# Kernel tuning notes

Hardware: AMD Instinct MI355X
Metric: run time of the kernel (lower is better)

## Reference

```python
import jax, jax.numpy as jnp
import numpy as np

NUM_HEADS = 16
ROTARY_BASE = 10000.0


def _apply_rotary(x):
    # x: (B, S, H, D); GPT-NeoX style rotate-half over full head dim
    B, S, H, D = x.shape
    half = D // 2
    inv_freq = 1.0 / (ROTARY_BASE ** (jnp.arange(0, half, dtype=jnp.float32) / half))
    t = jnp.arange(S, dtype=jnp.float32)
    freqs = jnp.einsum('s,d->sd', t, inv_freq)          # (S, half)
    cos = jnp.cos(freqs)[None, :, None, :]               # (1, S, 1, half)
    sin = jnp.sin(freqs)[None, :, None, :]
    x1, x2 = x[..., :half], x[..., half:]
    return jnp.concatenate([x1 * cos - x2 * sin, x2 * cos + x1 * sin], axis=-1).astype(x.dtype)


def setup_inputs() -> dict:
    key = jax.random.key(0)
    k0, k1, k2 = jax.random.split(key, 3)
    B, S, E = 2, 2048, 2048
    x = jax.random.normal(k0, (B, S, E), dtype=jnp.float32)
    wqkv = jax.random.normal(k1, (3 * E, E), dtype=jnp.float32) * 0.02
    bqkv = jnp.zeros((3 * E,), dtype=jnp.float32)
    wout = jax.random.normal(k2, (E, E), dtype=jnp.float32) * 0.02
    bout = jnp.zeros((E,), dtype=jnp.float32)
    return {"x": x, "wqkv": wqkv, "bqkv": bqkv, "wout": wout, "bout": bout}


def reference(x, wqkv, bqkv, wout, bout):
    B, S, E = x.shape
    H = NUM_HEADS
    D = E // H
    # fused QKV projection: (B, S, 3, H, D)
    qkv = (jnp.einsum('bse,fe->bsf', x, wqkv) + bqkv).reshape(B, S, 3, H, D)
    q, k, v = qkv[:, :, 0], qkv[:, :, 1], qkv[:, :, 2]
    q = _apply_rotary(q)
    k = _apply_rotary(k)
    scale = 1.0 / jnp.sqrt(jnp.float32(D))
    scores = jnp.einsum('bthd,bshd->bhts', q, k) * scale  # (B, H, S, S)
    causal_mask = jnp.triu(jnp.full((S, S), -10000.0, dtype=scores.dtype), 1)
    attn = jax.nn.softmax(scores + causal_mask, axis=-1)
    ctx = jnp.einsum('bhts,bshd->bthd', attn, v).reshape(B, S, E)
    return jnp.einsum('bse,fe->bsf', ctx, wout) + bout
```

## Files before the change

kernel.cpp:

```cpp
#include <hip/hip_runtime.h>
#include <math.h>

#define BB 2
#define SS 2048
#define EE 2048
#define HH 16
#define DD 128
#define FF 6144

typedef __attribute__((ext_vector_type(8))) short short8;
typedef __attribute__((ext_vector_type(4))) float floatx4;

static __device__ __forceinline__ unsigned short f2bf(float x) {
  unsigned u = __float_as_uint(x);
  u += 0x7fffu + ((u >> 16) & 1u);
  return (unsigned short)(u >> 16);
}
static __device__ __forceinline__ float bf2f(unsigned short h) {
  return __uint_as_float((unsigned)h << 16);
}

#define GLOAD_LDS16(gp, lp)                                       \
  __builtin_amdgcn_global_load_lds(                               \
      (const __attribute__((address_space(1))) void*)(gp),        \
      (__attribute__((address_space(3))) void*)(lp), 16, 0, 0)

__global__ __launch_bounds__(256) void cast_f32_bf16(
    const float* __restrict__ in, unsigned short* __restrict__ out, int n4) {
  const int i = blockIdx.x * 256 + threadIdx.x;
  if (i >= n4) return;
  const float4 v = ((const float4*)in)[i];
  ushort4 o;
  o.x = f2bf(v.x); o.y = f2bf(v.y); o.z = f2bf(v.z); o.w = f2bf(v.w);
  ((ushort4*)out)[i] = o;
}

static __device__ __forceinline__ void store_out(float* p, float v) { *p = v; }
static __device__ __forceinline__ void store_out(unsigned short* p, float v) {
  *p = f2bf(v);
}

template <typename OutT>
__global__ __launch_bounds__(256) void gemm_bf16_mfma(
    const unsigned short* __restrict__ A, const unsigned short* __restrict__ Bt,
    const float* __restrict__ bias, OutT* __restrict__ C,
    int M, int N, int K) {
  __shared__ unsigned short As[2][128][32];
  __shared__ unsigned short Bs[2][128][32];
  const int tid = threadIdx.x;
  const int L = tid & 63;
  const int w = tid >> 6;
  const int m0 = blockIdx.y * 128;
  const int n0 = blockIdx.x * 128;

  const int i0 = w * 2;
  const int lrow = L >> 2;
  const int lcol = (L & 3) * 8;
  const size_t a_off0 = (size_t)(m0 + (i0 + 0) * 16 + lrow) * K + lcol;
  const size_t a_off1 = (size_t)(m0 + (i0 + 1) * 16 + lrow) * K + lcol;
  const size_t b_off0 = (size_t)(n0 + (i0 + 0) * 16 + lrow) * K + lcol;
  const size_t b_off1 = (size_t)(n0 + (i0 + 1) * 16 + lrow) * K + lcol;

  const int wr = (w >> 1) * 64;
  const int wc = (w & 1) * 64;
  const int lane16 = L & 15;
  const int quad = L >> 4;

  floatx4 acc[4][4] = {};

  GLOAD_LDS16(A + a_off0, &As[0][(i0 + 0) * 16][0]);
  GLOAD_LDS16(A + a_off1, &As[0][(i0 + 1) * 16][0]);
  GLOAD_LDS16(Bt + b_off0, &Bs[0][(i0 + 0) * 16][0]);
  GLOAD_LDS16(Bt + b_off1, &Bs[0][(i0 + 1) * 16][0]);

  for (int k0 = 0; k0 < K; k0 += 32) {
    const int cur = (k0 >> 5) & 1;
    __syncthreads();
    if (k0 + 32 < K) {
      const int nxt = cur ^ 1;
      GLOAD_LDS16(A + a_off0 + k0 + 32, &As[nxt][(i0 + 0) * 16][0]);
      GLOAD_LDS16(A + a_off1 + k0 + 32, &As[nxt][(i0 + 1) * 16][0]);
      GLOAD_LDS16(Bt + b_off0 + k0 + 32, &Bs[nxt][(i0 + 0) * 16][0]);
      GLOAD_LDS16(Bt + b_off1 + k0 + 32, &Bs[nxt][(i0 + 1) * 16][0]);
    }

    short8 a[4], b[4];
#pragma unroll
    for (int mi = 0; mi < 4; ++mi)
      a[mi] = *(const short8*)(&As[cur][wr + mi * 16 + lane16][quad * 8]);
#pragma unroll
    for (int ni = 0; ni < 4; ++ni)
      b[ni] = *(const short8*)(&Bs[cur][wc + ni * 16 + lane16][quad * 8]);
#pragma unroll
    for (int mi = 0; mi < 4; ++mi)
#pragma unroll
      for (int ni = 0; ni < 4; ++ni)
        acc[mi][ni] = __builtin_amdgcn_mfma_f32_16x16x32_bf16(
            a[mi], b[ni], acc[mi][ni], 0, 0, 0);
  }

#pragma unroll
  for (int ni = 0; ni < 4; ++ni) {
    const int col = n0 + wc + ni * 16 + lane16;
    const float bv = bias[col];
#pragma unroll
    for (int mi = 0; mi < 4; ++mi) {
      const int row = m0 + wr + mi * 16 + quad * 4;
#pragma unroll
      for (int r = 0; r < 4; ++r)
        store_out(&C[(size_t)(row + r) * N + col], acc[mi][ni][r] + bv);
    }
  }
}

template <typename OutT>
__global__ __launch_bounds__(512, 2) void gemm_bf16_256x192(
    const unsigned short* __restrict__ A, const unsigned short* __restrict__ Bt,
    const float* __restrict__ bias, OutT* __restrict__ C,
    int M, int N, int K) {
  __shared__ __align__(16) unsigned short As[2][16384];
  __shared__ __align__(16) unsigned short Bs[2][12288];

  const int tid = threadIdx.x;
  const int w = tid >> 6;
  const int L = tid & 63;
  const int lane16 = L & 15;
  const int quad = L >> 4;
  const int wm = w >> 2;
  const int wn = w & 3;

  const int nby = M >> 8;
  const int q8 = gridDim.x >> 3;
  const int wg = (blockIdx.x & 7) * q8 + (blockIdx.x >> 3);
  const int by = wg % nby;
  const int bx = wg / nby;
  const int m0 = by << 8;
  const int n0 = bx * 192;

  const int lA = ((w >> 1) << 4) + (L >> 2);
  const int scol = ((w & 1) << 5) + (((L & 3) * 8) ^ ((L & 32) ? 16 : 0));
  unsigned aoff[4], boff[3];
#pragma unroll
  for (int j = 0; j < 4; ++j)
    aoff[j] = (unsigned)(m0 + j * 64 + lA) * (unsigned)K + scol;
#pragma unroll
  for (int j = 0; j < 3; ++j)
    boff[j] = (unsigned)(n0 + j * 64 + lA) * (unsigned)K + scol;
  const int ldst = w * 512;

  const int sq = (quad * 8) ^ ((lane16 & 8) << 1);
  const int rbase = lane16 * 32 + sq;

  floatx4 acc[8][3] = {};

  GLOAD_LDS16(A + aoff[0], &As[0][0 * 4096 + ldst]);
  GLOAD_LDS16(A + aoff[1], &As[0][1 * 4096 + ldst]);
  GLOAD_LDS16(A + aoff[2], &As[0][2 * 4096 + ldst]);
  GLOAD_LDS16(A + aoff[3], &As[0][3 * 4096 + ldst]);
  GLOAD_LDS16(Bt + boff[0], &Bs[0][0 * 4096 + ldst]);
  GLOAD_LDS16(Bt + boff[1], &Bs[0][1 * 4096 + ldst]);
  GLOAD_LDS16(Bt + boff[2], &Bs[0][2 * 4096 + ldst]);
  GLOAD_LDS16(Bt + boff[0] + 64, &Bs[1][0 * 4096 + ldst]);
  GLOAD_LDS16(Bt + boff[1] + 64, &Bs[1][1 * 4096 + ldst]);
  GLOAD_LDS16(Bt + boff[2] + 64, &Bs[1][2 * 4096 + ldst]);
  asm volatile("s_waitcnt vmcnt(3)" ::: "memory");
  __builtin_amdgcn_sched_barrier(0);
  __builtin_amdgcn_s_barrier();

  const int NT = K >> 6;
  short8 a[4][2], b[3][2];

  for (int t = 0; t < NT; ++t) {
    const int c = t & 1;
    const unsigned kn1 = (unsigned)(t + 1) << 6;
    const unsigned kn2 = (unsigned)(t + 2) << 6;
    const unsigned short* Ac = &As[c][0];
    const unsigned short* Bc = &Bs[c][0];

#pragma unroll
    for (int mi = 0; mi < 4; ++mi)
#pragma unroll
      for (int kk = 0; kk < 2; ++kk)
        a[mi][kk] = *(const short8*)(Ac + (wm * 2) * 4096 +
                                     ((mi * 2 + kk) * 512) + rbase);
#pragma unroll
    for (int ni = 0; ni < 3; ++ni) {
      const int f = wn * 3 + ni;
#pragma unroll
      for (int kk = 0; kk < 2; ++kk)
        b[ni][kk] = *(const short8*)(Bc + (f >> 2) * 4096 +
                                     (((f & 3) * 2 + kk) * 512) + rbase);
    }
    GLOAD_LDS16(A + aoff[0] + kn1, &As[c ^ 1][0 * 4096 + ldst]);
    GLOAD_LDS16(A + aoff[1] + kn1, &As[c ^ 1][1 * 4096 + ldst]);
    GLOAD_LDS16(A + aoff[2] + kn1, &As[c ^ 1][2 * 4096 + ldst]);
    GLOAD_LDS16(A + aoff[3] + kn1, &As[c ^ 1][3 * 4096 + ldst]);
    __builtin_amdgcn_s_setprio(1);
#pragma unroll
    for (int mi = 0; mi < 4; ++mi)
#pragma unroll
      for (int ni = 0; ni < 3; ++ni)
#pragma unroll
        for (int kk = 0; kk < 2; ++kk)
          acc[mi][ni] = __builtin_amdgcn_mfma_f32_16x16x32_bf16(
              a[mi][kk], b[ni][kk], acc[mi][ni], 0, 0, 0);
    __builtin_amdgcn_s_setprio(0);
    __builtin_amdgcn_sched_barrier(0);
    __builtin_amdgcn_s_barrier();

#pragma unroll
    for (int mi = 0; mi < 4; ++mi)
#pragma unroll
      for (int kk = 0; kk < 2; ++kk)
        a[mi][kk] = *(const short8*)(Ac + (wm * 2 + 1) * 4096 +
                                     ((mi * 2 + kk) * 512) + rbase);
    GLOAD_LDS16(Bt + boff[0] + kn2, &Bs[c][0 * 4096 + ldst]);
    GLOAD_LDS16(Bt + boff[1] + kn2, &Bs[c][1 * 4096 + ldst]);
    GLOAD_LDS16(Bt + boff[2] + kn2, &Bs[c][2 * 4096 + ldst]);
    __builtin_amdgcn_s_setprio(1);
#pragma unroll
    for (int mi = 0; mi < 4; ++mi)
#pragma unroll
      for (int ni = 0; ni < 3; ++ni)
#pragma unroll
        for (int kk = 0; kk < 2; ++kk)
          acc[4 + mi][ni] = __builtin_amdgcn_mfma_f32_16x16x32_bf16(
              a[mi][kk], b[ni][kk], acc[4 + mi][ni], 0, 0, 0);
    __builtin_amdgcn_s_setprio(0);
    asm volatile("s_waitcnt vmcnt(3)" ::: "memory");
    __builtin_amdgcn_sched_barrier(0);
    __builtin_amdgcn_s_barrier();
  }

#pragma unroll
  for (int ni = 0; ni < 3; ++ni) {
    const int col = n0 + wn * 48 + ni * 16 + lane16;
    const float bv = bias[col];
#pragma unroll
    for (int mi = 0; mi < 8; ++mi) {
      const int row = m0 + wm * 128 + mi * 16 + quad * 4;
#pragma unroll
      for (int r = 0; r < 4; ++r)
        store_out(&C[(size_t)(row + r) * N + col], acc[mi][ni][r] + bv);
    }
  }
}

__global__ __launch_bounds__(256) void rotary_kernel(unsigned short* __restrict__ qkv) {
  const int idx = blockIdx.x * blockDim.x + threadIdx.x;
  const int d = idx & 63;
  const int h = (idx >> 6) & (HH - 1);
  const int s = (idx >> 10) & (SS - 1);
  const int b = idx >> 21;

  const float inv_freq = __expf(-(float)d * 0.14391156509f);
  float sn, c;
  __sincosf((float)s * inv_freq, &sn, &c);

  const size_t base = ((size_t)b * SS + s) * FF + h * DD + d;
  unsigned short* q = qkv + base;
  unsigned short* k = qkv + base + EE;

  const float q1 = bf2f(q[0]), q2 = bf2f(q[64]);
  q[0]  = f2bf(q1 * c - q2 * sn);
  q[64] = f2bf(q2 * c + q1 * sn);
  const float k1 = bf2f(k[0]), k2 = bf2f(k[64]);
  k[0]  = f2bf(k1 * c - k2 * sn);
  k[64] = f2bf(k2 * c + k1 * sn);
}

__global__ __launch_bounds__(256) void transpose_v(
    const unsigned short* __restrict__ qkv, unsigned short* __restrict__ vt) {
  __shared__ unsigned short T[64][72];
  const int t = threadIdx.x;
  const int s0 = blockIdx.x * 64;
  const int d0 = blockIdx.y * 64;
  const int bh = blockIdx.z;
  const int b = bh >> 4, h = bh & 15;
  {
    const int r = t >> 2, c = (t & 3) * 16;
    const unsigned short* src =
        qkv + ((size_t)b * SS + s0 + r) * FF + 2 * EE + h * DD + d0 + c;
    const uint4 u0 = *(const uint4*)src;
    const uint4 u1 = *(const uint4*)(src + 8);
    *(uint4*)&T[r][c] = u0;
    *(uint4*)&T[r][c + 8] = u1;
  }
  __syncthreads();
  {
    const int rr = t >> 2, cc = (t & 3) * 16;
    unsigned short vals[16];
#pragma unroll
    for (int j = 0; j < 16; ++j) vals[j] = T[cc + j][rr];
    unsigned short* dst =
        vt + (size_t)bh * DD * SS + (size_t)(d0 + rr) * SS + s0 + cc;
    *(uint4*)dst = *(uint4*)&vals[0];
    *(uint4*)(dst + 8) = *(uint4*)&vals[8];
  }
}

#define ATQ 128
#define ATK 32
#define SPAD 40
#define NQT (SS / ATQ)

__global__ __launch_bounds__(256, 2) void attn_mfma(
    const unsigned short* __restrict__ qkv,
    const unsigned short* __restrict__ vt,
    unsigned short* __restrict__ ctx) {
  __shared__ __align__(16) unsigned short Ksh[2][ATK * DD];
  __shared__ __align__(16) unsigned short Vsh[2][DD * ATK];
  __shared__ __align__(16) unsigned short Ssh[ATQ][SPAD];

  const int tid = threadIdx.x;
  const int L = tid & 63;
  const int w = tid >> 6;
  const int lane16 = L & 15;
  const int quad = L >> 4;

  const int flat = blockIdx.x;
  const int bh_lin = flat & 31;
  const int qb = (NQT - 1) - (flat >> 5);
  const int b = bh_lin >> 4;
  const int h = bh_lin & 15;
  const int bh = b * HH + h;
  const float scale = 0.08838834764831845f;

  size_t koff[2], voff[2];
  int kdst[2], vdst[2];
#pragma unroll
  for (int j = 0; j < 2; ++j) {
    const int ck = j * 256 + tid;
    const int kk = ck >> 4;
    const int cgk = (ck & 15) ^ (kk & 15);
    koff[j] = ((size_t)b * SS + kk) * FF + EE + h * DD + cgk * 8;
    kdst[j] = (j * 256 + w * 64) * 8;
    const int d = ck >> 2;
    const int cgv = (ck & 3) ^ (d & 3);
    voff[j] = (size_t)bh * DD * SS + (size_t)d * SS + cgv * 8;
    vdst[j] = kdst[j];
  }

  const int q0 = qb * ATQ;

  short8 qf[2][4];
#pragma unroll
  for (int mi = 0; mi < 2; ++mi) {
    const int q = q0 + w * 32 + mi * 16 + lane16;
    const unsigned short* qp =
        qkv + ((size_t)b * SS + q) * FF + h * DD + quad * 8;
#pragma unroll
    for (int dc = 0; dc < 4; ++dc)
      qf[mi][dc] = *(const short8*)(qp + dc * 32);
  }

  floatx4 acc[8][2] = {};
  float m_i[2] = {-3.0e38f, -3.0e38f};
  float l_i[2] = {0.0f, 0.0f};

  const int nkt = 4 * qb + 4;
  const int mykt = 4 * qb + w;

#pragma unroll
  for (int j = 0; j < 2; ++j) {
    GLOAD_LDS16(qkv + koff[j], &Ksh[0][kdst[j]]);
    GLOAD_LDS16(vt + voff[j], &Vsh[0][vdst[j]]);
  }

  for (int kt = 0; kt < nkt; ++kt) {
    const int cur = kt & 1;
    __syncthreads();
    if (kt + 1 < nkt) {
      const size_t ka = (size_t)(kt + 1) * ATK * FF;
      const int va = (kt + 1) * ATK;
#pragma unroll
      for (int j = 0; j < 2; ++j) {
        GLOAD_LDS16(qkv + koff[j] + ka, &Ksh[cur ^ 1][kdst[j]]);
        GLOAD_LDS16(vt + voff[j] + va, &Vsh[cur ^ 1][vdst[j]]);
      }
    }
    if (kt > mykt) continue;
    const int k0 = kt * ATK;
    const unsigned short* Kc = Ksh[cur];
    const unsigned short* Vc = Vsh[cur];

    floatx4 st[2][2] = {};
    __builtin_amdgcn_s_setprio(1);
#pragma unroll
    for (int kkt = 0; kkt < 2; ++kkt) {
      const unsigned short* krow = Kc + (kkt * 16 + lane16) * 128;
#pragma unroll
      for (int dc = 0; dc < 4; ++dc) {
        const short8 kf =
            *(const short8*)(krow + ((dc * 4 + quad) ^ lane16) * 8);
#pragma unroll
        for (int mi = 0; mi < 2; ++mi)
          st[kkt][mi] = __builtin_amdgcn_mfma_f32_16x16x32_bf16(
              kf, qf[mi][dc], st[kkt][mi], 0, 0, 0);
      }
    }
    __builtin_amdgcn_s_setprio(0);

    const bool needmask = (kt == mykt);
#pragma unroll
    for (int mi = 0; mi < 2; ++mi) {
      const int q_glob = q0 + w * 32 + mi * 16 + lane16;
#pragma unroll
      for (int kkt = 0; kkt < 2; ++kkt) {
        const int kkb = k0 + kkt * 16 + quad * 4;
#pragma unroll
        for (int r = 0; r < 4; ++r) {
          float v = st[kkt][mi][r] * scale;
          if (needmask && (kkb + r) > q_glob) v = -3.0e38f;
          st[kkt][mi][r] = v;
        }
      }
    }

#pragma unroll
    for (int mi = 0; mi < 2; ++mi) {
      float tm = -3.0e38f;
#pragma unroll
      for (int kkt = 0; kkt < 2; ++kkt)
#pragma unroll
        for (int r = 0; r < 4; ++r) tm = fmaxf(tm, st[kkt][mi][r]);
      tm = fmaxf(tm, __shfl_xor(tm, 16));
      tm = fmaxf(tm, __shfl_xor(tm, 32));

      const bool need = !__all(tm - m_i[mi] <= 8.0f);
      if (need) {
        const float mn = fmaxf(m_i[mi], tm);
        const float alpha = __expf(m_i[mi] - mn);
        m_i[mi] = mn;
        l_i[mi] *= alpha;
#pragma unroll
        for (int dt = 0; dt < 8; ++dt)
#pragma unroll
          for (int r = 0; r < 4; ++r) acc[dt][mi][r] *= alpha;
      }

      float rs = 0.0f;
#pragma unroll
      for (int kkt = 0; kkt < 2; ++kkt)
#pragma unroll
        for (int r = 0; r < 4; ++r) {
          const float p = __expf(st[kkt][mi][r] - m_i[mi]);
          st[kkt][mi][r] = p;
          rs += p;
        }
      rs += __shfl_xor(rs, 16);
      rs += __shfl_xor(rs, 32);
      l_i[mi] += rs;

#pragma unroll
      for (int kkt = 0; kkt < 2; ++kkt) {
        ushort4 pk;
        pk.x = f2bf(st[kkt][mi][0]);
        pk.y = f2bf(st[kkt][mi][1]);
        pk.z = f2bf(st[kkt][mi][2]);
        pk.w = f2bf(st[kkt][mi][3]);
        *(ushort4*)(&Ssh[w * 32 + mi * 16 + lane16][kkt * 16 + quad * 4]) = pk;
      }
    }

    short8 pa[2];
#pragma unroll
    for (int mi = 0; mi < 2; ++mi)
      pa[mi] = *(const short8*)(&Ssh[w * 32 + mi * 16 + lane16][quad * 8]);
    const int vpos = (quad ^ (lane16 & 3)) * 8;
    __builtin_amdgcn_s_setprio(1);
#pragma unroll
    for (int dt = 0; dt < 8; ++dt) {
      const short8 vf = *(const short8*)(Vc + (dt * 16 + lane16) * 32 + vpos);
#pragma unroll
      for (int mi = 0; mi < 2; ++mi)
        acc[dt][mi] = __builtin_amdgcn_mfma_f32_16x16x32_bf16(
            vf, pa[mi], acc[dt][mi], 0, 0, 0);
    }
    __builtin_amdgcn_s_setprio(0);
  }

#pragma unroll
  for (int mi = 0; mi < 2; ++mi) {
    const float inv = 1.0f / l_i[mi];
    const int q = q0 + w * 32 + mi * 16 + lane16;
    unsigned short* op = ctx + ((size_t)b * SS + q) * EE + h * DD + quad * 4;
#pragma unroll
    for (int dt = 0; dt < 8; ++dt) {
      ushort4 o;
      o.x = f2bf(acc[dt][mi][0] * inv);
      o.y = f2bf(acc[dt][mi][1] * inv);
      o.z = f2bf(acc[dt][mi][2] * inv);
      o.w = f2bf(acc[dt][mi][3] * inv);
      *(ushort4*)(op + dt * 16) = o;
    }
  }
}

extern "C" void kernel_launch(void* const* d_in, const int* in_sizes, int n_in,
                              void* d_out, int out_size, void* d_ws,
                              size_t ws_size, hipStream_t stream) {
  const float* x    = (const float*)d_in[0];
  const float* wqkv = (const float*)d_in[1];
  const float* bqkv = (const float*)d_in[2];
  const float* wout = (const float*)d_in[3];
  const float* bout = (const float*)d_in[4];
  float* out = (float*)d_out;

  unsigned short* qkvb = (unsigned short*)d_ws;
  unsigned short* xb   = qkvb + (size_t)25165824;
  unsigned short* wqb  = xb + (size_t)8388608;
  unsigned short* ctxb = wqb + (size_t)12582912;
  unsigned short* wob  = ctxb + (size_t)8388608;
  unsigned short* vtb  = wob + (size_t)4194304;

  const int M = BB * SS;

  cast_f32_bf16<<<8192, 256, 0, stream>>>(x, xb, 2097152);
  cast_f32_bf16<<<12288, 256, 0, stream>>>(wqkv, wqb, 3145728);
  cast_f32_bf16<<<4096, 256, 0, stream>>>(wout, wob, 1048576);

  {
    gemm_bf16_256x192<unsigned short><<<dim3(512), 512, 0, stream>>>(
        xb, wqb, bqkv, qkvb, M, FF, EE);
  }
  {
    const int total = BB * SS * HH * 64;
    rotary_kernel<<<total / 256, 256, 0, stream>>>(qkvb);
  }
  {
    dim3 grid(SS / 64, DD / 64, BB * HH);
    transpose_v<<<grid, 256, 0, stream>>>(qkvb, vtb);
  }
  {
    attn_mfma<<<dim3(512), 256, 0, stream>>>(qkvb, vtb, ctxb);
  }
  {
    dim3 grid(EE / 128, M / 128);
    gemm_bf16_mfma<float><<<grid, 256, 0, stream>>>(
        ctxb, wob, bout, out, M, EE, EE);
  }
}
```

Baseline: 419.9 us.

## Use 512-thread attention with 16 rows per wave and a new 256x128 output GEMM

The attention kernel now runs 512 threads per block, each wave owning 16 query rows instead of 32, with one K/V load per thread per tile. The goal is more waves per CU and lower register pressure, at the cost of loading K/V fragments for fewer rows each. The output projection drops the simple 128x128 GEMM for a new 256x128 kernel with swizzled LDS, split-phase prefetch, grouped block ordering and setprio. That kernel should raise MFMA utilization on the 4096x2048x2048 GEMM.

Measured after the change: 398.3 us. -5.2%, faster.

```diff
diff --git a/kernel.cpp b/kernel.cpp
--- a/kernel.cpp
+++ b/kernel.cpp
@@ -38,79 +38,6 @@
 static __device__ __forceinline__ void store_out(float* p, float v) { *p = v; }
 static __device__ __forceinline__ void store_out(unsigned short* p, float v) {
   *p = f2bf(v);
-}
-
-template <typename OutT>
-__global__ __launch_bounds__(256) void gemm_bf16_mfma(
-    const unsigned short* __restrict__ A, const unsigned short* __restrict__ Bt,
-    const float* __restrict__ bias, OutT* __restrict__ C,
-    int M, int N, int K) {
-  __shared__ unsigned short As[2][128][32];
-  __shared__ unsigned short Bs[2][128][32];
-  const int tid = threadIdx.x;
-  const int L = tid & 63;
-  const int w = tid >> 6;
-  const int m0 = blockIdx.y * 128;
-  const int n0 = blockIdx.x * 128;
-
-  const int i0 = w * 2;
-  const int lrow = L >> 2;
-  const int lcol = (L & 3) * 8;
-  const size_t a_off0 = (size_t)(m0 + (i0 + 0) * 16 + lrow) * K + lcol;
-  const size_t a_off1 = (size_t)(m0 + (i0 + 1) * 16 + lrow) * K + lcol;
-  const size_t b_off0 = (size_t)(n0 + (i0 + 0) * 16 + lrow) * K + lcol;
-  const size_t b_off1 = (size_t)(n0 + (i0 + 1) * 16 + lrow) * K + lcol;
-
-  const int wr = (w >> 1) * 64;
-  const int wc = (w & 1) * 64;
-  const int lane16 = L & 15;
-  const int quad = L >> 4;
-
-  floatx4 acc[4][4] = {};
-
-  GLOAD_LDS16(A + a_off0, &As[0][(i0 + 0) * 16][0]);
-  GLOAD_LDS16(A + a_off1, &As[0][(i0 + 1) * 16][0]);
-  GLOAD_LDS16(Bt + b_off0, &Bs[0][(i0 + 0) * 16][0]);
-  GLOAD_LDS16(Bt + b_off1, &Bs[0][(i0 + 1) * 16][0]);
-
-  for (int k0 = 0; k0 < K; k0 += 32) {
-    const int cur = (k0 >> 5) & 1;
-    __syncthreads();
-    if (k0 + 32 < K) {
-      const int nxt = cur ^ 1;
-      GLOAD_LDS16(A + a_off0 + k0 + 32, &As[nxt][(i0 + 0) * 16][0]);
-      GLOAD_LDS16(A + a_off1 + k0 + 32, &As[nxt][(i0 + 1) * 16][0]);
-      GLOAD_LDS16(Bt + b_off0 + k0 + 32, &Bs[nxt][(i0 + 0) * 16][0]);
-      GLOAD_LDS16(Bt + b_off1 + k0 + 32, &Bs[nxt][(i0 + 1) * 16][0]);
-    }
-
-    short8 a[4], b[4];
-#pragma unroll
-    for (int mi = 0; mi < 4; ++mi)
-      a[mi] = *(const short8*)(&As[cur][wr + mi * 16 + lane16][quad * 8]);
-#pragma unroll
-    for (int ni = 0; ni < 4; ++ni)
-      b[ni] = *(const short8*)(&Bs[cur][wc + ni * 16 + lane16][quad * 8]);
-#pragma unroll
-    for (int mi = 0; mi < 4; ++mi)
-#pragma unroll
-      for (int ni = 0; ni < 4; ++ni)
-        acc[mi][ni] = __builtin_amdgcn_mfma_f32_16x16x32_bf16(
-            a[mi], b[ni], acc[mi][ni], 0, 0, 0);
-  }
-
-#pragma unroll
-  for (int ni = 0; ni < 4; ++ni) {
-    const int col = n0 + wc + ni * 16 + lane16;
-    const float bv = bias[col];
-#pragma unroll
-    for (int mi = 0; mi < 4; ++mi) {
-      const int row = m0 + wr + mi * 16 + quad * 4;
-#pragma unroll
-      for (int r = 0; r < 4; ++r)
-        store_out(&C[(size_t)(row + r) * N + col], acc[mi][ni][r] + bv);
-    }
-  }
 }
 
 template <typename OutT>
@@ -246,6 +173,136 @@
   }
 }
 
+template <typename OutT>
+__global__ __launch_bounds__(512, 2) void gemm_bf16_256x128(
+    const unsigned short* __restrict__ A, const unsigned short* __restrict__ Bt,
+    const float* __restrict__ bias, OutT* __restrict__ C,
+    int M, int N, int K) {
+  __shared__ __align__(16) unsigned short As[2][16384];
+  __shared__ __align__(16) unsigned short Bs[2][8192];
+
+  const int tid = threadIdx.x;
+  const int w = tid >> 6;
+  const int L = tid & 63;
+  const int lane16 = L & 15;
+  const int quad = L >> 4;
+  const int wm = w >> 2;
+  const int wn = w & 3;
+
+  const int nby = M >> 8;
+  const int q8 = gridDim.x >> 3;
+  const int wg = (blockIdx.x & 7) * q8 + (blockIdx.x >> 3);
+  const int by = wg % nby;
+  const int bx = wg / nby;
+  const int m0 = by << 8;
+  const int n0 = bx << 7;
+
+  const int lA = ((w >> 1) << 4) + (L >> 2);
+  const int scol = ((w & 1) << 5) + (((L & 3) * 8) ^ ((L & 32) ? 16 : 0));
+  unsigned aoff[4], boff[2];
+#pragma unroll
+  for (int j = 0; j < 4; ++j)
+    aoff[j] = (unsigned)(m0 + j * 64 + lA) * (unsigned)K + scol;
+#pragma unroll
+  for (int j = 0; j < 2; ++j)
+    boff[j] = (unsigned)(n0 + j * 64 + lA) * (unsigned)K + scol;
+  const int ldst = w * 512;
+
+  const int sq = (quad * 8) ^ ((lane16 & 8) << 1);
+  const int rbase = lane16 * 32 + sq;
+
+  floatx4 acc[8][2] = {};
+
+  GLOAD_LDS16(A + aoff[0], &As[0][0 * 4096 + ldst]);
+  GLOAD_LDS16(A + aoff[1], &As[0][1 * 4096 + ldst]);
+  GLOAD_LDS16(A + aoff[2], &As[0][2 * 4096 + ldst]);
+  GLOAD_LDS16(A + aoff[3], &As[0][3 * 4096 + ldst]);
+  GLOAD_LDS16(Bt + boff[0], &Bs[0][0 * 4096 + ldst]);
+  GLOAD_LDS16(Bt + boff[1], &Bs[0][1 * 4096 + ldst]);
+  GLOAD_LDS16(Bt + boff[0] + 64, &Bs[1][0 * 4096 + ldst]);
+  GLOAD_LDS16(Bt + boff[1] + 64, &Bs[1][1 * 4096 + ldst]);
+  asm volatile("s_waitcnt vmcnt(2)" ::: "memory");
+  __builtin_amdgcn_sched_barrier(0);
+  __builtin_amdgcn_s_barrier();
+
+  const int NT = K >> 6;
+  short8 a[4][2], b[2][2];
+
+  for (int t = 0; t < NT; ++t) {
+    const int c = t & 1;
+    const unsigned kn1 = (unsigned)(t + 1) << 6;
+    const unsigned kn2 = (unsigned)(t + 2) << 6;
+    const unsigned short* Ac = &As[c][0];
+    const unsigned short* Bc = &Bs[c][0];
+
+#pragma unroll
+    for (int mi = 0; mi < 4; ++mi)
+#pragma unroll
+      for (int kk = 0; kk < 2; ++kk)
+        a[mi][kk] = *(const short8*)(Ac + (wm * 2) * 4096 +
+                                     ((mi * 2 + kk) * 512) + rbase);
+#pragma unroll
+    for (int ni = 0; ni < 2; ++ni) {
+      const int f = wn * 2 + ni;
+#pragma unroll
+      for (int kk = 0; kk < 2; ++kk)
+        b[ni][kk] = *(const short8*)(Bc + (f >> 2) * 4096 +
+                                     (((f & 3) * 2 + kk) * 512) + rbase);
+    }
+    GLOAD_LDS16(A + aoff[0] + kn1, &As[c ^ 1][0 * 4096 + ldst]);
+    GLOAD_LDS16(A + aoff[1] + kn1, &As[c ^ 1][1 * 4096 + ldst]);
+    GLOAD_LDS16(A + aoff[2] + kn1, &As[c ^ 1][2 * 4096 + ldst]);
+    GLOAD_LDS16(A + aoff[3] + kn1, &As[c ^ 1][3 * 4096 + ldst]);
+    __builtin_amdgcn_s_setprio(1);
+#pragma unroll
+    for (int mi = 0; mi < 4; ++mi)
+#pragma unroll
+      for (int ni = 0; ni < 2; ++ni)
+#pragma unroll
+        for (int kk = 0; kk < 2; ++kk)
+          acc[mi][ni] = __builtin_amdgcn_mfma_f32_16x16x32_bf16(
+              a[mi][kk], b[ni][kk], acc[mi][ni], 0, 0, 0);
+    __builtin_amdgcn_s_setprio(0);
+    __builtin_amdgcn_sched_barrier(0);
+    __builtin_amdgcn_s_barrier();
+
+#pragma unroll
+    for (int mi = 0; mi < 4; ++mi)
+#pragma unroll
+      for (int kk = 0; kk < 2; ++kk)
+        a[mi][kk] = *(const short8*)(Ac + (wm * 2 + 1) * 4096 +
+                                     ((mi * 2 + kk) * 512) + rbase);
+    GLOAD_LDS16(Bt + boff[0] + kn2, &Bs[c][0 * 4096 + ldst]);
+    GLOAD_LDS16(Bt + boff[1] + kn2, &Bs[c][1 * 4096 + ldst]);
+    __builtin_amdgcn_s_setprio(1);
+#pragma unroll
+    for (int mi = 0; mi < 4; ++mi)
+#pragma unroll
+      for (int ni = 0; ni < 2; ++ni)
+#pragma unroll
+        for (int kk = 0; kk < 2; ++kk)
+          acc[4 + mi][ni] = __builtin_amdgcn_mfma_f32_16x16x32_bf16(
+              a[mi][kk], b[ni][kk], acc[4 + mi][ni], 0, 0, 0);
+    __builtin_amdgcn_s_setprio(0);
+    asm volatile("s_waitcnt vmcnt(2)" ::: "memory");
+    __builtin_amdgcn_sched_barrier(0);
+    __builtin_amdgcn_s_barrier();
+  }
+
+#pragma unroll
+  for (int ni = 0; ni < 2; ++ni) {
+    const int col = n0 + wn * 32 + ni * 16 + lane16;
+    const float bv = bias[col];
+#pragma unroll
+    for (int mi = 0; mi < 8; ++mi) {
+      const int row = m0 + wm * 128 + mi * 16 + quad * 4;
+#pragma unroll
+      for (int r = 0; r < 4; ++r)
+        store_out(&C[(size_t)(row + r) * N + col], acc[mi][ni][r] + bv);
+    }
+  }
+}
+
 __global__ __launch_bounds__(256) void rotary_kernel(unsigned short* __restrict__ qkv) {
   const int idx = blockIdx.x * blockDim.x + threadIdx.x;
   const int d = idx & 63;
@@ -304,7 +361,7 @@
 #define SPAD 40
 #define NQT (SS / ATQ)
 
-__global__ __launch_bounds__(256, 2) void attn_mfma(
+__global__ __launch_bounds__(512, 4) void attn_mfma(
     const unsigned short* __restrict__ qkv,
     const unsigned short* __restrict__ vt,
     unsigned short* __restrict__ ctx) {
@@ -326,46 +383,35 @@
   const int bh = b * HH + h;
   const float scale = 0.08838834764831845f;
 
-  size_t koff[2], voff[2];
-  int kdst[2], vdst[2];
-#pragma unroll
-  for (int j = 0; j < 2; ++j) {
-    const int ck = j * 256 + tid;
-    const int kk = ck >> 4;
-    const int cgk = (ck & 15) ^ (kk & 15);
-    koff[j] = ((size_t)b * SS + kk) * FF + EE + h * DD + cgk * 8;
-    kdst[j] = (j * 256 + w * 64) * 8;
-    const int d = ck >> 2;
-    const int cgv = (ck & 3) ^ (d & 3);
-    voff[j] = (size_t)bh * DD * SS + (size_t)d * SS + cgv * 8;
-    vdst[j] = kdst[j];
-  }
+  const int kkrow = tid >> 4;
+  const int cgk = (tid & 15) ^ (kkrow & 15);
+  const size_t koff =
+      ((size_t)b * SS + kkrow) * FF + EE + h * DD + cgk * 8;
+  const int drow = tid >> 2;
+  const int cgv = (tid & 3) ^ (drow & 3);
+  const size_t voff = (size_t)bh * DD * SS + (size_t)drow * SS + cgv * 8;
+  const int dstKV = w * 512;
 
   const int q0 = qb * ATQ;
 
-  short8 qf[2][4];
-#pragma unroll
-  for (int mi = 0; mi < 2; ++mi) {
-    const int q = q0 + w * 32 + mi * 16 + lane16;
+  short8 qf[4];
+  {
+    const int q = q0 + w * 16 + lane16;
     const unsigned short* qp =
         qkv + ((size_t)b * SS + q) * FF + h * DD + quad * 8;
 #pragma unroll
-    for (int dc = 0; dc < 4; ++dc)
-      qf[mi][dc] = *(const short8*)(qp + dc * 32);
-  }
-
-  floatx4 acc[8][2] = {};
-  float m_i[2] = {-3.0e38f, -3.0e38f};
-  float l_i[2] = {0.0f, 0.0f};
+    for (int dc = 0; dc < 4; ++dc) qf[dc] = *(const short8*)(qp + dc * 32);
+  }
+
+  floatx4 acc[8] = {};
+  float m_i = -3.0e38f;
+  float l_i = 0.0f;
 
   const int nkt = 4 * qb + 4;
-  const int mykt = 4 * qb + w;
-
-#pragma unroll
-  for (int j = 0; j < 2; ++j) {
-    GLOAD_LDS16(qkv + koff[j], &Ksh[0][kdst[j]]);
-    GLOAD_LDS16(vt + voff[j], &Vsh[0][vdst[j]]);
-  }
+  const int mykt = 4 * qb + (w >> 1);
+
+  GLOAD_LDS16(qkv + koff, &Ksh[0][dstKV]);
+  GLOAD_LDS16(vt + voff, &Vsh[0][dstKV]);
 
   for (int kt = 0; kt < nkt; ++kt) {
     const int cur = kt & 1;
@@ -373,18 +419,15 @@
     if (kt + 1 < nkt) {
       const size_t ka = (size_t)(kt + 1) * ATK * FF;
       const int va = (kt + 1) * ATK;
-#pragma unroll
-      for (int j = 0; j < 2; ++j) {
-        GLOAD_LDS16(qkv + koff[j] + ka, &Ksh[cur ^ 1][kdst[j]]);
-        GLOAD_LDS16(vt + voff[j] + va, &Vsh[cur ^ 1][vdst[j]]);
-      }
+      GLOAD_LDS16(qkv + koff + ka, &Ksh[cur ^ 1][dstKV]);
+      GLOAD_LDS16(vt + voff + va, &Vsh[cur ^ 1][dstKV]);
     }
     if (kt > mykt) continue;
     const int k0 = kt * ATK;
     const unsigned short* Kc = Ksh[cur];
     const unsigned short* Vc = Vsh[cur];
 
-    floatx4 st[2][2] = {};
+    floatx4 st[2] = {};
     __builtin_amdgcn_s_setprio(1);
 #pragma unroll
     for (int kkt = 0; kkt < 2; ++kkt) {
@@ -393,50 +436,44 @@
       for (int dc = 0; dc < 4; ++dc) {
         const short8 kf =
             *(const short8*)(krow + ((dc * 4 + quad) ^ lane16) * 8);
-#pragma unroll
-        for (int mi = 0; mi < 2; ++mi)
-          st[kkt][mi] = __builtin_amdgcn_mfma_f32_16x16x32_bf16(
-              kf, qf[mi][dc], st[kkt][mi], 0, 0, 0);
+        st[kkt] = __builtin_amdgcn_mfma_f32_16x16x32_bf16(
+            kf, qf[dc], st[kkt], 0, 0, 0);
       }
     }
     __builtin_amdgcn_s_setprio(0);
 
     const bool needmask = (kt == mykt);
-#pragma unroll
-    for (int mi = 0; mi < 2; ++mi) {
-      const int q_glob = q0 + w * 32 + mi * 16 + lane16;
-#pragma unroll
-      for (int kkt = 0; kkt < 2; ++kkt) {
-        const int kkb = k0 + kkt * 16 + quad * 4;
-#pragma unroll
-        for (int r = 0; r < 4; ++r) {
-          float v = st[kkt][mi][r] * scale;
-          if (needmask && (kkb + r) > q_glob) v = -3.0e38f;
-          st[kkt][mi][r] = v;
-        }
+    const int q_glob = q0 + w * 16 + lane16;
+#pragma unroll
+    for (int kkt = 0; kkt < 2; ++kkt) {
+      const int kkb = k0 + kkt * 16 + quad * 4;
+#pragma unroll
+      for (int r = 0; r < 4; ++r) {
+        float v = st[kkt][r] * scale;
+        if (needmask && (kkb + r) > q_glob) v = -3.0e38f;
+        st[kkt][r] = v;
       }
     }
 
-#pragma unroll
-    for (int mi = 0; mi < 2; ++mi) {
+    {
       float tm = -3.0e38f;
 #pragma unroll
       for (int kkt = 0; kkt < 2; ++kkt)
 #pragma unroll
-        for (int r = 0; r < 4; ++r) tm = fmaxf(tm, st[kkt][mi][r]);
+        for (int r = 0; r < 4; ++r) tm = fmaxf(tm, st[kkt][r]);
       tm = fmaxf(tm, __shfl_xor(tm, 16));
       tm = fmaxf(tm, __shfl_xor(tm, 32));
 
-      const bool need = !__all(tm - m_i[mi] <= 8.0f);
+      const bool need = !__all(tm - m_i <= 8.0f);
       if (need) {
-        const float mn = fmaxf(m_i[mi], tm);
-        const float alpha = __expf(m_i[mi] - mn);
-        m_i[mi] = mn;
-        l_i[mi] *= alpha;
+        const float mn = fmaxf(m_i, tm);
+        const float alpha = __expf(m_i - mn);
+        m_i = mn;
+        l_i *= alpha;
 #pragma unroll
         for (int dt = 0; dt < 8; ++dt)
 #pragma unroll
-          for (int r = 0; r < 4; ++r) acc[dt][mi][r] *= alpha;
+          for (int r = 0; r < 4; ++r) acc[dt][r] *= alpha;
       }
 
       float rs = 0.0f;
@@ -444,54 +481,49 @@
       for (int kkt = 0; kkt < 2; ++kkt)
 #pragma unroll
         for (int r = 0; r < 4; ++r) {
-          const float p = __expf(st[kkt][mi][r] - m_i[mi]);
-          st[kkt][mi][r] = p;
+          const float p = __expf(st[kkt][r] - m_i);
+          st[kkt][r] = p;
           rs += p;
         }
       rs += __shfl_xor(rs, 16);
       rs += __shfl_xor(rs, 32);
-      l_i[mi] += rs;
+      l_i += rs;
 
 #pragma unroll
       for (int kkt = 0; kkt < 2; ++kkt) {
         ushort4 pk;
-        pk.x = f2bf(st[kkt][mi][0]);
-        pk.y = f2bf(st[kkt][mi][1]);
-        pk.z = f2bf(st[kkt][mi][2]);
-        pk.w = f2bf(st[kkt][mi][3]);
-        *(ushort4*)(&Ssh[w * 32 + mi * 16 + lane16][kkt * 16 + quad * 4]) = pk;
+        pk.x = f2bf(st[kkt][0]);
+        pk.y = f2bf(st[kkt][1]);
+        pk.z = f2bf(st[kkt][2]);
+        pk.w = f2bf(st[kkt][3]);
+        *(ushort4*)(&Ssh[w * 16 + lane16][kkt * 16 + quad * 4]) = pk;
       }
     }
 
-    short8 pa[2];
-#pragma unroll
-    for (int mi = 0; mi < 2; ++mi)
-      pa[mi] = *(const short8*)(&Ssh[w * 32 + mi * 16 + lane16][quad * 8]);
+    const short8 pa =
+        *(const short8*)(&Ssh[w * 16 + lane16][quad * 8]);
     const int vpos = (quad ^ (lane16 & 3)) * 8;
     __builtin_amdgcn_s_setprio(1);
 #pragma unroll
     for (int dt = 0; dt < 8; ++dt) {
       const short8 vf = *(const short8*)(Vc + (dt * 16 + lane16) * 32 + vpos);
-#pragma unroll
-      for (int mi = 0; mi < 2; ++mi)
-        acc[dt][mi] = __builtin_amdgcn_mfma_f32_16x16x32_bf16(
-            vf, pa[mi], acc[dt][mi], 0, 0, 0);
+      acc[dt] = __builtin_amdgcn_mfma_f32_16x16x32_bf16(
+          vf, pa, acc[dt], 0, 0, 0);
     }
     __builtin_amdgcn_s_setprio(0);
   }
 
-#pragma unroll
-  for (int mi = 0; mi < 2; ++mi) {
-    const float inv = 1.0f / l_i[mi];
-    const int q = q0 + w * 32 + mi * 16 + lane16;
+  {
+    const float inv = 1.0f / l_i;
+    const int q = q0 + w * 16 + lane16;
     unsigned short* op = ctx + ((size_t)b * SS + q) * EE + h * DD + quad * 4;
 #pragma unroll
     for (int dt = 0; dt < 8; ++dt) {
       ushort4 o;
-      o.x = f2bf(acc[dt][mi][0] * inv);
-      o.y = f2bf(acc[dt][mi][1] * inv);
-      o.z = f2bf(acc[dt][mi][2] * inv);
-      o.w = f2bf(acc[dt][mi][3] * inv);
+      o.x = f2bf(acc[dt][0] * inv);
+      o.y = f2bf(acc[dt][1] * inv);
+      o.z = f2bf(acc[dt][2] * inv);
+      o.w = f2bf(acc[dt][3] * inv);
       *(ushort4*)(op + dt * 16) = o;
     }
   }
@@ -533,11 +565,10 @@
     transpose_v<<<grid, 256, 0, stream>>>(qkvb, vtb);
   }
   {
-    attn_mfma<<<dim3(512), 256, 0, stream>>>(qkvb, vtb, ctxb);
-  }
-  {
-    dim3 grid(EE / 128, M / 128);
-    gemm_bf16_mfma<float><<<grid, 256, 0, stream>>>(
+    attn_mfma<<<dim3(512), 512, 0, stream>>>(qkvb, vtb, ctxb);
+  }
+  {
+    gemm_bf16_256x128<float><<<dim3(256), 512, 0, stream>>>(
         ctxb, wob, bout, out, M, EE, EE);
   }
 }
```
